# Kernel tuning notes

Measured on AMD Instinct MI355X. Metric: run time of the kernel, lower is better.

Reference implementation:

```python
import jax, jax.numpy as jnp
import numpy as np

N = 32                      # rotation matrix size (n x n)
INPUT_DIM = 512
HIDDEN = 1024
BATCH = 16384
NUM_ANGLES = N * (N - 1) // 2   # 496

# Givens plane indices in the same order as the original double loop:
# i = 0..n-2, j = i+1..n-1 (row-major upper triangle)
_I_IDX, _J_IDX = np.triu_indices(N, k=1)


def setup_inputs() -> dict:
    key = jax.random.key(0)
    k0, k1, k2 = jax.random.split(key, 3)
    x = jax.random.normal(k0, (BATCH, INPUT_DIM), dtype=jnp.float32)
    # nn.Linear weights: fc (hidden, input_dim), fc2 (num_angles, hidden)
    W1 = jax.random.normal(k1, (HIDDEN, INPUT_DIM), dtype=jnp.float32) / np.sqrt(INPUT_DIM)
    b1 = jnp.zeros((HIDDEN,), dtype=jnp.float32)
    W2 = jax.random.normal(k2, (NUM_ANGLES, HIDDEN), dtype=jnp.float32) / np.sqrt(HIDDEN)
    b2 = jnpups = jnp.zeros((NUM_ANGLES,), dtype=jnp.float32)
    return {"x": x, "W1": W1, "b1": b1, "W2": W2, "b2": b2}


def reference(x, W1, b1, W2, b2):
    """Faithful forward: MLP -> angles -> sequential Givens-rotation product.

    Right-multiplying R by the Givens matrix G(i, j, theta) only mixes
    columns i and j of R, so each loop iteration is a 2-column update
    instead of a full [B, n, n] bmm. Same math as the original.
    """
    B = x.shape[0]
    h = jax.nn.relu(x @ W1.T + b1)                 # [B, HIDDEN]
    angles = jnp.mod(h @ W2.T + b2, 2.0 * jnp.pi)  # [B, NUM_ANGLES]
    c_all = jnp.cos(angles).T                      # [A, B]
    s_all = jnp.sin(angles).T                      # [A, B]

    R0 = jnp.tile(jnp.eye(N, dtype=x.dtype), (B, 1, 1))  # [B, n, n]
    i_idx = jnp.asarray(_I_IDX)
    j_idx = jnp.asarray(_J_IDX)

    def step(R, inp):
        i, j, c, s = inp                # scalars i, j; c, s: [B]
        col_i = R[:, :, i]              # [B, n]
        col_j = R[:, :, j]              # [B, n]
        new_i = col_i * c[:, None] + col_j * s[:, None]
        new_j = -col_i * s[:, None] + col_j * c[:, None]
        R = R.at[:, :, i].set(new_i)
        R = R.at[:, :, j].set(new_j)
        return R, None

    R, _ = jax.lax.scan(step, R0, (i_idx, j_idx, c_all, s_all))
    return R
```

## Files before the change

### kernel.cpp

```cpp
#include <hip/hip_runtime.h>
#include <math.h>
#include <utility>

#define BATCH 16384
#define INPUT_DIM 512
#define HIDDEN 1024
#define NROT 32
#define NANG 496

typedef _Float16 half8 __attribute__((ext_vector_type(8)));
typedef float    f32x4 __attribute__((ext_vector_type(4)));

__global__ __launch_bounds__(256) void cvt_f32_f16(
    const float* __restrict__ src, _Float16* __restrict__ dst, int n8)
{
    const int i = blockIdx.x * 256 + threadIdx.x;
    if (i < n8) {
        const float4* s = (const float4*)src + (size_t)i * 2;
        const float4 a = s[0], b = s[1];
        half8 h;
        h[0]=(_Float16)a.x; h[1]=(_Float16)a.y; h[2]=(_Float16)a.z; h[3]=(_Float16)a.w;
        h[4]=(_Float16)b.x; h[5]=(_Float16)b.y; h[6]=(_Float16)b.z; h[7]=(_Float16)b.w;
        *(half8*)(dst + (size_t)i * 8) = h;
    }
}

template<int EPI>
__global__ __launch_bounds__(256) void gemm_nt_f16(
    const _Float16* __restrict__ A, const _Float16* __restrict__ B,
    const float* __restrict__ bias, float* __restrict__ Cf,
    _Float16* __restrict__ Ch, int M, int N, int K, int Nout)
{
    constexpr int BK = 32;
    __shared__ _Float16 sA[2][128 * BK];
    __shared__ _Float16 sB[2][128 * BK];

    const int tid = threadIdx.x;
    const int m0 = blockIdx.y * 128;
    const int n0 = blockIdx.x * 128;

    const int rA  = tid >> 2;
    const int k8  = tid & 3;
    const int swW = ((k8 ^ (rA & 3)) << 3);

    half8 rg[4];

    auto load_tile = [&](int kt) {
        const size_t koff = (size_t)kt * BK + k8 * 8;
        rg[0] = *(const half8*)(A + (size_t)(m0 + rA) * K + koff);
        rg[1] = *(const half8*)(A + (size_t)(m0 + rA + 64) * K + koff);
        half8 z;
        #pragma unroll
        for (int j = 0; j < 8; ++j) z[j] = (_Float16)0.f;
        if (EPI == 0 || (n0 + rA) < N)
            rg[2] = *(const half8*)(B + (size_t)(n0 + rA) * K + koff);
        else rg[2] = z;
        if (EPI == 0 || (n0 + rA + 64) < N)
            rg[3] = *(const half8*)(B + (size_t)(n0 + rA + 64) * K + koff);
        else rg[3] = z;
    };

    auto write_tile = [&](int buf) {
        *(half8*)&sA[buf][ rA       * BK + swW] = rg[0];
        *(half8*)&sA[buf][(rA + 64) * BK + swW] = rg[1];
        *(half8*)&sB[buf][ rA       * BK + swW] = rg[2];
        *(half8*)&sB[buf][(rA + 64) * BK + swW] = rg[3];
    };

    const int lane = tid & 63;
    const int wid  = tid >> 6;
    const int wr = wid >> 1, wc = wid & 1;
    const int fr = lane & 15, fq = lane >> 4;
    const int swR   = ((fq ^ (fr & 3)) << 3);
    const int aBase = (wr * 64 + fr) * BK + swR;
    const int bBase = (wc * 64 + fr) * BK + swR;

    f32x4 acc[4][4];
    #pragma unroll
    for (int i = 0; i < 4; ++i)
        #pragma unroll
        for (int j = 0; j < 4; ++j) acc[i][j] = (f32x4)(0.f);

    const int NT = K / BK;
    load_tile(0);
    write_tile(0);
    int cur = 0;

    for (int kt = 0; kt < NT; ++kt) {
        const bool more = (kt + 1 < NT);
        if (more) load_tile(kt + 1);
        __syncthreads();

        half8 a_[4], b_[4];
        #pragma unroll
        for (int f = 0; f < 4; ++f) {
            a_[f] = *(const half8*)&sA[cur][aBase + f * 16 * BK];
            b_[f] = *(const half8*)&sB[cur][bBase + f * 16 * BK];
        }
        #pragma unroll
        for (int fm = 0; fm < 4; ++fm)
            #pragma unroll
            for (int fn = 0; fn < 4; ++fn)
                acc[fm][fn] = __builtin_amdgcn_mfma_f32_16x16x32_f16(
                    a_[fm], b_[fn], acc[fm][fn], 0, 0, 0);

        if (more) write_tile(cur ^ 1);
        cur ^= 1;
    }

    if (EPI == 0) {
        #pragma unroll
        for (int fn = 0; fn < 4; ++fn) {
            const int col = n0 + wc * 64 + fn * 16 + fr;
            const float bv = bias[col];
            #pragma unroll
            for (int fm = 0; fm < 4; ++fm) {
                const int row0 = m0 + wr * 64 + fm * 16 + fq * 4;
                #pragma unroll
                for (int r = 0; r < 4; ++r)
                    Ch[(size_t)(row0 + r) * Nout + col] =
                        (_Float16)fmaxf(acc[fm][fn][r] + bv, 0.f);
            }
        }
    } else {
        #pragma unroll
        for (int fn = 0; fn < 4; ++fn) {
            const int col = n0 + wc * 64 + fn * 16 + fr;
            if (col < Nout) {
                const float bv = bias[col];
                #pragma unroll
                for (int fm = 0; fm < 4; ++fm) {
                    const int row0 = m0 + wr * 64 + fm * 16 + fq * 4;
                    #pragma unroll
                    for (int r = 0; r < 4; ++r) {
                        const float ang = acc[fm][fn][r] + bv;
                        float s, c;
                        __sincosf(ang, &s, &c);
                        *(float2*)(Cf + ((size_t)(row0 + r) * Nout + col) * 2) =
                            make_float2(c, s);
                    }
                }
            }
        }
    }
}

struct IJTbl { unsigned char i[NANG]; unsigned char j[NANG]; };
constexpr IJTbl make_ij_tbl() {
    IJTbl t{};
    int k = 0;
    for (int i = 0; i < NROT - 1; ++i)
        for (int j = i + 1; j < NROT; ++j) { t.i[k] = (unsigned char)i; t.j[k] = (unsigned char)j; ++k; }
    return t;
}
constexpr IJTbl IJT = make_ij_tbl();

template<int M>
__device__ __forceinline__ void rot_pair(const f32x4 q, float (&v)[NROT]) {
    {
        constexpr int k = 2 * M;
        constexpr int i = IJT.i[k], j = IJT.j[k];
        const float vi = v[i], vj = v[j];
        v[i] = fmaf(q[0], vi,  q[1] * vj);
        v[j] = fmaf(q[0], vj, -q[1] * vi);
    }
    {
        constexpr int k = 2 * M + 1;
        constexpr int i = IJT.i[k], j = IJT.j[k];
        const float vi = v[i], vj = v[j];
        v[i] = fmaf(q[2], vi,  q[3] * vj);
        v[j] = fmaf(q[2], vj, -q[3] * vi);
    }
}

template<int W, int T>
__device__ __forceinline__ void chain_grp(const float* __restrict__ lcs,
                                          float (&v)[NROT]) {
    const f32x4 q = *(const f32x4*)(lcs + (62 * W + T) * 4);
    rot_pair<62 * W + T>(q, v);
}

template<int W, size_t... Ts>
__device__ __forceinline__ void chain_runW(const float* __restrict__ lcs,
                                           float (&v)[NROT],
                                           std::index_sequence<Ts...>) {
    (chain_grp<W, (int)Ts>(lcs, v), ...);
}

#define LROW_H 4096
#define RT_H   8192
#define PL_H   12288
#define PRT_H  14336

template<int W>
__device__ __forceinline__ void chain_and_store(const float* __restrict__ lcs,
                                                _Float16* __restrict__ lh,
                                                int half, int r) {
    float v[NROT];
    #pragma unroll
    for (int c = 0; c < NROT; ++c) v[c] = (c == r) ? 1.f : 0.f;
    chain_runW<W>(lcs, v, std::make_index_sequence<62>{});

    if constexpr ((W & 1) == 0) {
        const int base = LROW_H + (half * 2 + (W >> 1)) * 1024;
        #pragma unroll
        for (int kq = 0; kq < 4; ++kq) {
            half8 hv;
            #pragma unroll
            for (int j = 0; j < 8; ++j) hv[j] = (_Float16)v[kq * 8 + j];
            *(half8*)&lh[base + r * 32 + ((kq ^ (r & 3)) << 3)] = hv;
        }
    } else {
        const int base = RT_H + (half * 2 + (W >> 1)) * 1024;
        #pragma unroll
        for (int c = 0; c < NROT; ++c)
            lh[base + c * 32 + (((r >> 3) ^ (c & 3)) << 3) + (r & 7)] =
                (_Float16)v[c];
    }
}

__global__ __launch_bounds__(256) void rotate_kernel(
    const float4* __restrict__ cs4, float* __restrict__ out)
{
    __shared__ float smem[8192];
    _Float16* lh = (_Float16*)smem;

    const int tid  = threadIdx.x;
    const int wid  = tid >> 6;
    const int lane = tid & 63;
    const int half = (tid >> 5) & 1;
    const int r    = tid & 31;
    const int fr = lane & 15, fq = lane >> 4;
    const size_t b0 = (size_t)blockIdx.x * 2;

    float4* l4 = (float4*)smem;
    #pragma unroll
    for (int t = 0; t < 2; ++t) {
        const int idx = t * 256 + tid;
        if (idx < 496) {
            const int ba = idx >= 248;
            const int m  = idx - ba * 248;
            l4[ba * 248 + m] = cs4[(b0 + ba) * 248 + m];
        }
    }
    __syncthreads();

    const float* lcs = smem + half * 992;
    if      (wid == 0) chain_and_store<0>(lcs, lh, half, r);
    else if (wid == 1) chain_and_store<1>(lcs, lh, half, r);
    else if (wid == 2) chain_and_store<2>(lcs, lh, half, r);
    else               chain_and_store<3>(lcs, lh, half, r);
    __syncthreads();

    {
        const int ba = wid >> 1, pi = wid & 1;
        const int Ab = LROW_H + (ba * 2 + pi) * 1024;
        const int Bb = RT_H   + (ba * 2 + pi) * 1024;
        half8 a[2], b[2];
        #pragma unroll
        for (int mi = 0; mi < 2; ++mi) {
            a[mi] = *(const half8*)&lh[Ab + (mi * 16 + fr) * 32 + ((fq ^ (fr & 3)) << 3)];
            b[mi] = *(const half8*)&lh[Bb + (mi * 16 + fr) * 32 + ((fq ^ (fr & 3)) << 3)];
        }
        f32x4 d[2][2];
        #pragma unroll
        for (int mi = 0; mi < 2; ++mi)
            #pragma unroll
            for (int ni = 0; ni < 2; ++ni)
                d[mi][ni] = __builtin_amdgcn_mfma_f32_16x16x32_f16(
                    a[mi], b[ni], (f32x4)(0.f), 0, 0, 0);

        if (pi == 0) {
            const int base = PL_H + ba * 1024;
            #pragma unroll
            for (int mi = 0; mi < 2; ++mi)
                #pragma unroll
                for (int ni = 0; ni < 2; ++ni)
                    #pragma unroll
                    for (int q = 0; q < 4; ++q) {
                        const int row = mi * 16 + fq * 4 + q;
                        const int col = ni * 16 + fr;
                        lh[base + row * 32 + (((col >> 3) ^ (row & 3)) << 3) + (col & 7)] =
                            (_Float16)d[mi][ni][q];
                    }
        } else {
            const int base = PRT_H + ba * 1024;
            #pragma unroll
            for (int mi = 0; mi < 2; ++mi)
                #pragma unroll
                for (int ni = 0; ni < 2; ++ni)
                    #pragma unroll
                    for (int q = 0; q < 4; ++q) {
                        const int row = mi * 16 + fq * 4 + q;
                        const int col = ni * 16 + fr;
                        lh[base + col * 32 + (((row >> 3) ^ (col & 3)) << 3) + (row & 7)] =
                            (_Float16)d[mi][ni][q];
                    }
        }
    }
    __syncthreads();

    {
        const int ba = wid >> 1, mi = wid & 1;
        const int Ab = PL_H  + ba * 1024;
        const int Bb = PRT_H + ba * 1024;
        const half8 a = *(const half8*)&lh[Ab + (mi * 16 + fr) * 32 + ((fq ^ (fr & 3)) << 3)];
        #pragma unroll
        for (int ni = 0; ni < 2; ++ni) {
            const half8 b = *(const half8*)&lh[Bb + (ni * 16 + fr) * 32 + ((fq ^ (fr & 3)) << 3)];
            const f32x4 d = __builtin_amdgcn_mfma_f32_16x16x32_f16(
                a, b, (f32x4)(0.f), 0, 0, 0);
            #pragma unroll
            for (int q = 0; q < 4; ++q) {
                const int row = mi * 16 + fq * 4 + q;
                const int col = ni * 16 + fr;
                smem[ba * 1024 + row * 32 + (((col >> 2) ^ (row & 7)) << 2) + (col & 3)] = d[q];
            }
        }
    }
    __syncthreads();

    #pragma unroll
    for (int s = 0; s < 2; ++s) {
        const int idx = s * 256 + tid;
        const int ba  = idx >> 8;
        const int f4i = idx & 255;
        const int row = f4i >> 3;
        const int cc  = f4i & 7;
        const f32x4 val = *(const f32x4*)&smem[ba * 1024 + row * 32 + ((cc ^ (row & 7)) << 2)];
        *(f32x4*)(out + (b0 + ba) * 1024 + (size_t)f4i * 4) = val;
    }
}

extern "C" void kernel_launch(void* const* d_in, const int* in_sizes, int n_in,
                              void* d_out, int out_size, void* d_ws, size_t ws_size,
                              hipStream_t stream)
{
    const float* x  = (const float*)d_in[0];
    const float* W1 = (const float*)d_in[1];
    const float* b1 = (const float*)d_in[2];
    const float* W2 = (const float*)d_in[3];
    const float* b2 = (const float*)d_in[4];
    float* out = (float*)d_out;

    _Float16* h16  = (_Float16*)d_out;
    _Float16* x16  = h16  + (size_t)BATCH * HIDDEN;
    _Float16* W116 = x16  + (size_t)BATCH * INPUT_DIM;
    _Float16* W216 = W116 + (size_t)HIDDEN * INPUT_DIM;
    float*    cs   = (float*)d_ws;

    cvt_f32_f16<<<dim3((BATCH * INPUT_DIM / 8 + 255) / 256), 256, 0, stream>>>(
        x, x16, BATCH * INPUT_DIM / 8);
    cvt_f32_f16<<<dim3((HIDDEN * INPUT_DIM / 8 + 255) / 256), 256, 0, stream>>>(
        W1, W116, HIDDEN * INPUT_DIM / 8);
    cvt_f32_f16<<<dim3((NANG * HIDDEN / 8 + 255) / 256), 256, 0, stream>>>(
        W2, W216, NANG * HIDDEN / 8);

    gemm_nt_f16<0><<<dim3(HIDDEN / 128, BATCH / 128), 256, 0, stream>>>(
        x16, W116, b1, nullptr, h16, BATCH, HIDDEN, INPUT_DIM, HIDDEN);

    gemm_nt_f16<1><<<dim3((NANG + 127) / 128, BATCH / 128), 256, 0, stream>>>(
        h16, W216, b2, cs, nullptr, BATCH, NANG, HIDDEN, NANG);

    rotate_kernel<<<dim3(BATCH / 2), 256, 0, stream>>>(
        (const float4*)cs, out);
}
```

Before: 124.0 us.

## Store raw angles, compute sincos in rotate kernel, transpose-free odd chunks

The angle GEMM epilogue now writes only the raw angle instead of interleaved cos/sin pairs, which halves the intermediate workspace traffic. The sin/cos evaluation moves into the rotate kernel's load phase. Odd-numbered rotation chunks now apply their Givens steps in reverse order with transposed signs. This yields the transpose of the partial product, so every chunk can be stored row-major and the combining MFMAs swap operands instead of using strided scalar LDS writes. The shared memory footprint also shrinks, which may raise occupancy, but the element-wise half4 stores and the reordered swizzles carry a risk of correctness or bank-conflict issues.

```diff
diff --git a/kernel.cpp b/kernel.cpp
--- a/kernel.cpp
+++ b/kernel.cpp
@@ -9,6 +9,7 @@
 #define NANG 496
 
 typedef _Float16 half8 __attribute__((ext_vector_type(8)));
+typedef _Float16 half4 __attribute__((ext_vector_type(4)));
 typedef float    f32x4 __attribute__((ext_vector_type(4)));
 
 __global__ __launch_bounds__(256) void cvt_f32_f16(
@@ -132,13 +133,8 @@
                 for (int fm = 0; fm < 4; ++fm) {
                     const int row0 = m0 + wr * 64 + fm * 16 + fq * 4;
                     #pragma unroll
-                    for (int r = 0; r < 4; ++r) {
-                        const float ang = acc[fm][fn][r] + bv;
-                        float s, c;
-                        __sincosf(ang, &s, &c);
-                        *(float2*)(Cf + ((size_t)(row0 + r) * Nout + col) * 2) =
-                            make_float2(c, s);
-                    }
+                    for (int r = 0; r < 4; ++r)
+                        Cf[(size_t)(row0 + r) * Nout + col] = acc[fm][fn][r] + bv;
                 }
             }
         }
@@ -155,8 +151,13 @@
 }
 constexpr IJTbl IJT = make_ij_tbl();
 
+#define EVEN_H 4096
+#define ODD_H  8192
+#define PCM_H  0
+#define RF32   2048
+
 template<int M>
-__device__ __forceinline__ void rot_pair(const f32x4 q, float (&v)[NROT]) {
+__device__ __forceinline__ void rot_fwd(const f32x4 q, float (&v)[NROT]) {
     {
         constexpr int k = 2 * M;
         constexpr int i = IJT.i[k], j = IJT.j[k];
@@ -173,24 +174,44 @@
     }
 }
 
+template<int M>
+__device__ __forceinline__ void rot_rev(const f32x4 q, float (&v)[NROT]) {
+    {
+        constexpr int k = 2 * M + 1;
+        constexpr int i = IJT.i[k], j = IJT.j[k];
+        const float vi = v[i], vj = v[j];
+        v[i] = fmaf(q[2], vi, -q[3] * vj);
+        v[j] = fmaf(q[2], vj,  q[3] * vi);
+    }
+    {
+        constexpr int k = 2 * M;
+        constexpr int i = IJT.i[k], j = IJT.j[k];
+        const float vi = v[i], vj = v[j];
+        v[i] = fmaf(q[0], vi, -q[1] * vj);
+        v[j] = fmaf(q[0], vj,  q[1] * vi);
+    }
+}
+
 template<int W, int T>
-__device__ __forceinline__ void chain_grp(const float* __restrict__ lcs,
-                                          float (&v)[NROT]) {
-    const f32x4 q = *(const f32x4*)(lcs + (62 * W + T) * 4);
-    rot_pair<62 * W + T>(q, v);
+__device__ __forceinline__ void chain_step(const float* __restrict__ lcs,
+                                           float (&v)[NROT]) {
+    if constexpr ((W & 1) == 0) {
+        constexpr int fi = 62 * W + T;
+        const f32x4 q = *(const f32x4*)(lcs + fi * 4);
+        rot_fwd<fi>(q, v);
+    } else {
+        constexpr int fi = 62 * W + (61 - T);
+        const f32x4 q = *(const f32x4*)(lcs + fi * 4);
+        rot_rev<fi>(q, v);
+    }
 }
 
 template<int W, size_t... Ts>
 __device__ __forceinline__ void chain_runW(const float* __restrict__ lcs,
                                            float (&v)[NROT],
                                            std::index_sequence<Ts...>) {
-    (chain_grp<W, (int)Ts>(lcs, v), ...);
-}
-
-#define LROW_H 4096
-#define RT_H   8192
-#define PL_H   12288
-#define PRT_H  14336
+    (chain_step<W, (int)Ts>(lcs, v), ...);
+}
 
 template<int W>
 __device__ __forceinline__ void chain_and_store(const float* __restrict__ lcs,
@@ -201,28 +222,21 @@
     for (int c = 0; c < NROT; ++c) v[c] = (c == r) ? 1.f : 0.f;
     chain_runW<W>(lcs, v, std::make_index_sequence<62>{});
 
-    if constexpr ((W & 1) == 0) {
-        const int base = LROW_H + (half * 2 + (W >> 1)) * 1024;
-        #pragma unroll
-        for (int kq = 0; kq < 4; ++kq) {
-            half8 hv;
-            #pragma unroll
-            for (int j = 0; j < 8; ++j) hv[j] = (_Float16)v[kq * 8 + j];
-            *(half8*)&lh[base + r * 32 + ((kq ^ (r & 3)) << 3)] = hv;
-        }
-    } else {
-        const int base = RT_H + (half * 2 + (W >> 1)) * 1024;
-        #pragma unroll
-        for (int c = 0; c < NROT; ++c)
-            lh[base + c * 32 + (((r >> 3) ^ (c & 3)) << 3) + (r & 7)] =
-                (_Float16)v[c];
+    constexpr int REG = ((W & 1) == 0) ? EVEN_H : ODD_H;
+    const int base = REG + (half * 2 + (W >> 1)) * 1024;
+    #pragma unroll
+    for (int kq = 0; kq < 4; ++kq) {
+        half8 hv;
+        #pragma unroll
+        for (int j = 0; j < 8; ++j) hv[j] = (_Float16)v[kq * 8 + j];
+        *(half8*)&lh[base + r * 32 + ((kq ^ (r & 3)) << 3)] = hv;
     }
 }
 
 __global__ __launch_bounds__(256) void rotate_kernel(
-    const float4* __restrict__ cs4, float* __restrict__ out)
+    const float* __restrict__ theta, float* __restrict__ out)
 {
-    __shared__ float smem[8192];
+    __shared__ float smem[6144];
     _Float16* lh = (_Float16*)smem;
 
     const int tid  = threadIdx.x;
@@ -233,15 +247,16 @@
     const int fr = lane & 15, fq = lane >> 4;
     const size_t b0 = (size_t)blockIdx.x * 2;
 
-    float4* l4 = (float4*)smem;
-    #pragma unroll
-    for (int t = 0; t < 2; ++t) {
-        const int idx = t * 256 + tid;
-        if (idx < 496) {
-            const int ba = idx >= 248;
-            const int m  = idx - ba * 248;
-            l4[ba * 248 + m] = cs4[(b0 + ba) * 248 + m];
-        }
+    if (tid < 248) {
+        const f32x4 th = *(const f32x4*)(theta + b0 * NANG + tid * 4);
+        f32x4 p0, p1;
+        float s, c;
+        __sincosf(th[0], &s, &c); p0[0] = c; p0[1] = s;
+        __sincosf(th[1], &s, &c); p0[2] = c; p0[3] = s;
+        __sincosf(th[2], &s, &c); p1[0] = c; p1[1] = s;
+        __sincosf(th[3], &s, &c); p1[2] = c; p1[3] = s;
+        *(f32x4*)&smem[tid * 8]     = p0;
+        *(f32x4*)&smem[tid * 8 + 4] = p1;
     }
     __syncthreads();
 
@@ -254,68 +269,48 @@
 
     {
         const int ba = wid >> 1, pi = wid & 1;
-        const int Ab = LROW_H + (ba * 2 + pi) * 1024;
-        const int Bb = RT_H   + (ba * 2 + pi) * 1024;
+        const int Eb = EVEN_H + (ba * 2 + pi) * 1024;
+        const int Ob = ODD_H  + (ba * 2 + pi) * 1024;
+        const int Asrc = (pi == 0) ? Ob : Eb;
+        const int Bsrc = (pi == 0) ? Eb : Ob;
+        const int swz = (fq ^ (fr & 3)) << 3;
         half8 a[2], b[2];
         #pragma unroll
         for (int mi = 0; mi < 2; ++mi) {
-            a[mi] = *(const half8*)&lh[Ab + (mi * 16 + fr) * 32 + ((fq ^ (fr & 3)) << 3)];
-            b[mi] = *(const half8*)&lh[Bb + (mi * 16 + fr) * 32 + ((fq ^ (fr & 3)) << 3)];
-        }
-        f32x4 d[2][2];
+            a[mi] = *(const half8*)&lh[Asrc + (mi * 16 + fr) * 32 + swz];
+            b[mi] = *(const half8*)&lh[Bsrc + (mi * 16 + fr) * 32 + swz];
+        }
+        const int Pb = PCM_H + (ba * 2 + pi) * 1024;
         #pragma unroll
         for (int mi = 0; mi < 2; ++mi)
             #pragma unroll
-            for (int ni = 0; ni < 2; ++ni)
-                d[mi][ni] = __builtin_amdgcn_mfma_f32_16x16x32_f16(
+            for (int ni = 0; ni < 2; ++ni) {
+                const f32x4 d = __builtin_amdgcn_mfma_f32_16x16x32_f16(
                     a[mi], b[ni], (f32x4)(0.f), 0, 0, 0);
-
-        if (pi == 0) {
-            const int base = PL_H + ba * 1024;
-            #pragma unroll
-            for (int mi = 0; mi < 2; ++mi)
+                half4 hv;
                 #pragma unroll
-                for (int ni = 0; ni < 2; ++ni)
-                    #pragma unroll
-                    for (int q = 0; q < 4; ++q) {
-                        const int row = mi * 16 + fq * 4 + q;
-                        const int col = ni * 16 + fr;
-                        lh[base + row * 32 + (((col >> 3) ^ (row & 3)) << 3) + (col & 7)] =
-                            (_Float16)d[mi][ni][q];
-                    }
-        } else {
-            const int base = PRT_H + ba * 1024;
-            #pragma unroll
-            for (int mi = 0; mi < 2; ++mi)
-                #pragma unroll
-                for (int ni = 0; ni < 2; ++ni)
-                    #pragma unroll
-                    for (int q = 0; q < 4; ++q) {
-                        const int row = mi * 16 + fq * 4 + q;
-                        const int col = ni * 16 + fr;
-                        lh[base + col * 32 + (((row >> 3) ^ (col & 3)) << 3) + (row & 7)] =
-                            (_Float16)d[mi][ni][q];
-                    }
-        }
+                for (int q = 0; q < 4; ++q) hv[q] = (_Float16)d[q];
+                const int col  = ni * 16 + fr;
+                const int rowb = (mi * 16 + fq * 4) ^ ((col & 3) << 3);
+                *(half4*)&lh[Pb + col * 32 + rowb] = hv;
+            }
     }
     __syncthreads();
 
     {
         const int ba = wid >> 1, mi = wid & 1;
-        const int Ab = PL_H  + ba * 1024;
-        const int Bb = PRT_H + ba * 1024;
-        const half8 a = *(const half8*)&lh[Ab + (mi * 16 + fr) * 32 + ((fq ^ (fr & 3)) << 3)];
+        const int Ab = PCM_H + (ba * 2 + 1) * 1024;
+        const int Bb = PCM_H + (ba * 2 + 0) * 1024;
+        const int swz = (fq ^ (fr & 3)) << 3;
+        const half8 a = *(const half8*)&lh[Ab + (mi * 16 + fr) * 32 + swz];
         #pragma unroll
         for (int ni = 0; ni < 2; ++ni) {
-            const half8 b = *(const half8*)&lh[Bb + (ni * 16 + fr) * 32 + ((fq ^ (fr & 3)) << 3)];
+            const half8 b = *(const half8*)&lh[Bb + (ni * 16 + fr) * 32 + swz];
             const f32x4 d = __builtin_amdgcn_mfma_f32_16x16x32_f16(
                 a, b, (f32x4)(0.f), 0, 0, 0);
-            #pragma unroll
-            for (int q = 0; q < 4; ++q) {
-                const int row = mi * 16 + fq * 4 + q;
-                const int col = ni * 16 + fr;
-                smem[ba * 1024 + row * 32 + (((col >> 2) ^ (row & 7)) << 2) + (col & 3)] = d[q];
-            }
+            const int row  = ni * 16 + fr;
+            const int colq = mi * 4 + fq;
+            *(f32x4*)&smem[RF32 + ba * 1024 + row * 32 + ((colq ^ (row & 7)) << 2)] = d;
         }
     }
     __syncthreads();
@@ -327,7 +322,8 @@
         const int f4i = idx & 255;
         const int row = f4i >> 3;
         const int cc  = f4i & 7;
-        const f32x4 val = *(const f32x4*)&smem[ba * 1024 + row * 32 + ((cc ^ (row & 7)) << 2)];
+        const f32x4 val =
+            *(const f32x4*)&smem[RF32 + ba * 1024 + row * 32 + ((cc ^ (row & 7)) << 2)];
         *(f32x4*)(out + (b0 + ba) * 1024 + (size_t)f4i * 4) = val;
     }
 }
@@ -347,7 +343,7 @@
     _Float16* x16  = h16  + (size_t)BATCH * HIDDEN;
     _Float16* W116 = x16  + (size_t)BATCH * INPUT_DIM;
     _Float16* W216 = W116 + (size_t)HIDDEN * INPUT_DIM;
-    float*    cs   = (float*)d_ws;
+    float*    th   = (float*)d_ws;
 
     cvt_f32_f16<<<dim3((BATCH * INPUT_DIM / 8 + 255) / 256), 256, 0, stream>>>(
         x, x16, BATCH * INPUT_DIM / 8);
@@ -360,8 +356,7 @@
         x16, W116, b1, nullptr, h16, BATCH, HIDDEN, INPUT_DIM, HIDDEN);
 
     gemm_nt_f16<1><<<dim3((NANG + 127) / 128, BATCH / 128), 256, 0, stream>>>(
-        h16, W216, b2, cs, nullptr, BATCH, NANG, HIDDEN, NANG);
-
-    rotate_kernel<<<dim3(BATCH / 2), 256, 0, stream>>>(
-        (const float4*)cs, out);
-}
+        h16, W216, b2, th, nullptr, BATCH, NANG, HIDDEN, NANG);
+
+    rotate_kernel<<<dim3(BATCH / 2), 256, 0, stream>>>(th, out);
+}
```

Result: faster. 119.5 us (-3.7%).
